# Performance work log

Measured on AMD Instinct MI355X. Metric: run time of the kernel, lower is better.

Reference implementation:

```python
import jax, jax.numpy as jnp
import numpy as np

N, D_IN, D_OUT = 100000, 256, 256
R, E, B = 8, 40000, 4
LN_EPS = 1e-5


def setup_inputs() -> dict:
    key = jax.random.key(0)
    ks = jax.random.split(key, 6)
    x = jax.random.normal(ks[0], (N, D_IN), dtype=jnp.float32)
    edge_index = jax.random.randint(ks[1], (R, 2, E), 0, N, dtype=jnp.int64)
    bases = jax.random.normal(ks[2], (B, D_IN, D_OUT), dtype=jnp.float32) * 0.01
    coefficients = jax.random.normal(ks[3], (R, B), dtype=jnp.float32) * 0.01
    bound = 1.0 / np.sqrt(D_IN)
    w_self = jax.random.uniform(ks[4], (D_IN, D_OUT), minval=-bound, maxval=bound, dtype=jnp.float32)
    b_self = jax.random.uniform(ks[5], (D_OUT,), minval=-bound, maxval=bound, dtype=jnp.float32)
    ln_gamma = jnp.ones((D_OUT,), dtype=jnp.float32)
    ln_beta = jnp.zeros((D_OUT,), dtype=jnp.float32)
    return {"x": x, "edge_index": edge_index, "bases": bases,
            "coefficients": coefficients, "w_self": w_self, "b_self": b_self,
            "ln_gamma": ln_gamma, "ln_beta": ln_beta}


def reference(x, edge_index, bases, coefficients, w_self, b_self, ln_gamma, ln_beta):
    n = x.shape[0]
    # self loop
    h = x @ w_self + b_self                                   # (N, D_OUT)
    # basis-composed per-relation weights
    W = jnp.einsum('rb,bio->rio', coefficients, bases)        # (R, D_IN, D_OUT)
    src = edge_index[:, 0]                                    # (R, E)
    dst = edge_index[:, 1]                                    # (R, E)
    msg = jnp.einsum('red,rdo->reo', x[src], W)               # (R, E, D_OUT)
    seg = jax.vmap(lambda d, m: jax.ops.segment_sum(m, d, num_segments=n))(dst, msg)
    deg = jax.vmap(lambda d: jax.ops.segment_sum(jnp.ones(d.shape, x.dtype), d, num_segments=n))(dst)
    deg = jnp.maximum(deg, 1.0)                               # clamp(min=1)
    h = h + (seg / deg[..., None]).sum(axis=0)
    # LayerNorm(SiLU(h)); dropout is identity in eval
    a = jax.nn.silu(h)
    mean = a.mean(axis=-1, keepdims=True)
    var = ((a - mean) ** 2).mean(axis=-1, keepdims=True)
    return (a - mean) * jax.lax.rsqrt(var + LN_EPS) * ln_gamma + ln_beta
```

## Files before the change

kernel.cpp:

```cpp
#include <hip/hip_runtime.h>
#include <hip/hip_bf16.h>

#define N_NODES 100000
#define D 256
#define R_REL 8
#define E_EDGES 40000
#define LN_EPS 1e-5f
#define ETOT (R_REL * E_EDGES)
#define SCAN_CH 1024
#define SCAN_NB ((N_NODES + SCAN_CH - 1) / SCAN_CH)
#define NROWT ((N_NODES + 127) / 128)
#define NWG (NROWT * 10)
#define PREPX_NB (N_NODES * D / 8 / 256)
#define PREPB_NB 80
#define COUNT_NB ((ETOT + 255) / 256)

typedef __attribute__((ext_vector_type(8))) short short8;
typedef __attribute__((ext_vector_type(4))) float f32x4;
typedef __attribute__((ext_vector_type(2))) float f32x2;
typedef unsigned char uchar;

__device__ inline ushort bf16u(float f) {
    __hip_bfloat16 h = __float2bfloat16(f);
    return *reinterpret_cast<ushort*>(&h);
}
__device__ inline float bf2f(ushort u) { return __uint_as_float(((unsigned)u) << 16); }

__global__ __launch_bounds__(256) void k_prep(const float* __restrict__ x,
                                              ushort* __restrict__ xb,
                                              const float* __restrict__ w_self,
                                              const float* __restrict__ bases,
                                              ushort* __restrict__ BT,
                                              const int* __restrict__ ei,
                                              int* __restrict__ cntR) {
    __shared__ float tile[64][65];
    int b = blockIdx.x;
    int t = threadIdx.x;
    if (b < PREPX_NB) {
        size_t idx = (size_t)b * 256 + t;
        const float4* xp = (const float4*)(x + idx * 8);
        float4 f0 = xp[0], f1 = xp[1];
        short8 v;
        v[0] = (short)bf16u(f0.x); v[1] = (short)bf16u(f0.y);
        v[2] = (short)bf16u(f0.z); v[3] = (short)bf16u(f0.w);
        v[4] = (short)bf16u(f1.x); v[5] = (short)bf16u(f1.y);
        v[6] = (short)bf16u(f1.z); v[7] = (short)bf16u(f1.w);
        *(short8*)(xb + idx * 8) = v;
    } else if (b < PREPX_NB + PREPB_NB) {
        int bb = b - PREPX_NB;
        int ot = bb >> 2, dt = bb & 3;
        int o0 = ot * 64, d0 = dt * 64;
        int m = o0 >> 8;
        const float* src = (m == 0) ? w_self : bases + (size_t)(m - 1) * D * D;
        int ol0 = o0 & 255;
        int cl = t & 63, rw = t >> 6;
        for (int i = 0; i < 16; ++i) {
            int dl = i * 4 + rw;
            tile[dl][cl] = src[(size_t)(d0 + dl) * D + ol0 + cl];
        }
        __syncthreads();
        for (int i = 0; i < 16; ++i) {
            int ol = i * 4 + rw;
            BT[(size_t)(o0 + ol) * D + d0 + cl] = bf16u(tile[cl][ol]);
        }
    } else {
        int idx = (b - PREPX_NB - PREPB_NB) * 256 + t;
        if (idx < ETOT) {
            int r = idx / E_EDGES, e = idx % E_EDGES;
            int dst = ei[(r * 2 + 1) * E_EDGES + e];
            atomicAdd(&cntR[(size_t)dst * 8 + r], 1);
        }
    }
}

__global__ __launch_bounds__(256) void k_scanA(const int* __restrict__ cntR,
                                               int* __restrict__ start,
                                               int* __restrict__ sumsA) {
    __shared__ int sc[256];
    int t = threadIdx.x;
    int base = blockIdx.x * SCAN_CH + t * 4;
    int v[4];
#pragma unroll
    for (int i = 0; i < 4; ++i) {
        int node = base + i;
        int s = 0;
        if (node < N_NODES) {
            const int4* c = (const int4*)&cntR[(size_t)node * 8];
            int4 a = c[0], b = c[1];
            s = a.x + a.y + a.z + a.w + b.x + b.y + b.z + b.w;
        }
        v[i] = s;
    }
    int ts = v[0] + v[1] + v[2] + v[3];
    sc[t] = ts;
    __syncthreads();
    for (int off = 1; off < 256; off <<= 1) {
        int val = (t >= off) ? sc[t - off] : 0;
        __syncthreads();
        sc[t] += val;
        __syncthreads();
    }
    int excl = sc[t] - ts;
    if (base + 0 < N_NODES) start[base + 0] = excl;
    if (base + 1 < N_NODES) start[base + 1] = excl + v[0];
    if (base + 2 < N_NODES) start[base + 2] = excl + v[0] + v[1];
    if (base + 3 < N_NODES) start[base + 3] = excl + v[0] + v[1] + v[2];
    if (t == 255) sumsA[blockIdx.x] = sc[255];
}

__global__ __launch_bounds__(256) void k_scanB(const int* __restrict__ sumsA,
                                               int* __restrict__ sumsB) {
    __shared__ int sc[256];
    int t = threadIdx.x;
    int i0 = t * 4;
    int v0 = (i0 + 0 < SCAN_NB) ? sumsA[i0 + 0] : 0;
    int v1 = (i0 + 1 < SCAN_NB) ? sumsA[i0 + 1] : 0;
    int v2 = (i0 + 2 < SCAN_NB) ? sumsA[i0 + 2] : 0;
    int v3 = (i0 + 3 < SCAN_NB) ? sumsA[i0 + 3] : 0;
    int ts = v0 + v1 + v2 + v3;
    sc[t] = ts;
    __syncthreads();
    for (int off = 1; off < 256; off <<= 1) {
        int val = (t >= off) ? sc[t - off] : 0;
        __syncthreads();
        sc[t] += val;
        __syncthreads();
    }
    int excl = sc[t] - ts;
    if (i0 + 0 < SCAN_NB) sumsB[i0 + 0] = excl;
    if (i0 + 1 < SCAN_NB) sumsB[i0 + 1] = excl + v0;
    if (i0 + 2 < SCAN_NB) sumsB[i0 + 2] = excl + v0 + v1;
    if (i0 + 3 < SCAN_NB) sumsB[i0 + 3] = excl + v0 + v1 + v2;
}

__global__ __launch_bounds__(256) void k_scanC(int* __restrict__ start,
                                               const int* __restrict__ sumsB,
                                               int* __restrict__ cursor) {
    int idx = blockIdx.x * blockDim.x + threadIdx.x;
    if (idx < N_NODES) {
        int v = start[idx] + sumsB[idx / SCAN_CH];
        start[idx] = v;
        cursor[idx] = v;
    }
    if (idx == 0) start[N_NODES] = ETOT;
}

__global__ void k_scatter(const int* __restrict__ ei, int* __restrict__ cursor,
                          const int* __restrict__ cntR, int2* __restrict__ pairs) {
    int idx = blockIdx.x * blockDim.x + threadIdx.x;
    if (idx >= ETOT) return;
    int r = idx / E_EDGES, e = idx % E_EDGES;
    int src = ei[r * 2 * E_EDGES + e];
    int dst = ei[(r * 2 + 1) * E_EDGES + e];
    int pos = atomicAdd(&cursor[dst], 1);
    float invd = __builtin_amdgcn_rcpf((float)cntR[(size_t)dst * 8 + r]) * 0.015625f;
    pairs[pos] = make_int2((r << 20) | src, __float_as_int(invd));
}

__global__ __launch_bounds__(256, 2) void k_gemm(const ushort* __restrict__ xb,
                                                 const ushort* __restrict__ BT,
                                                 ushort* __restrict__ hb,
                                                 uchar* __restrict__ U) {
    __shared__ ushort As[2][128 * 64];
    __shared__ ushort Bs[2][128 * 64];
    int t = threadIdx.x;

    const int q = NWG / 8, r8 = NWG % 8;
    int dd = blockIdx.x;
    int xcd = dd & 7, slot = dd >> 3;
    int wgid = (xcd < r8 ? xcd * (q + 1) : r8 * (q + 1) + (xcd - r8) * q) + slot;
    int rowtile = wgid / 10, pass = wgid % 10;
    int row0 = rowtile * 128;

    int l = t & 63, w = t >> 6;
    int wr = w >> 1, wc = w & 1;
    int lr = l & 15, lg = l >> 4;

    auto stageA = [&](int buf, int kt) {
#pragma unroll
        for (int p = 0; p < 4; ++p) {
            int o = p * 4096 + t * 16;
            int rowA = o >> 7;
            int colb = (o & 127) ^ ((rowA & 7) << 4);
            int srcrow = min(row0 + rowA, N_NODES - 1);
            const char* gp = (const char*)xb + ((size_t)srcrow * D + kt * 64) * 2 + colb;
            char* lp = (char*)&As[buf][0] + p * 4096 + (t >> 6) * 1024;
            __builtin_amdgcn_global_load_lds(
                (const __attribute__((address_space(1))) void*)gp,
                (__attribute__((address_space(3))) void*)lp, 16, 0, 0);
        }
    };
    auto stageB = [&](int buf, int kt) {
#pragma unroll
        for (int p = 0; p < 4; ++p) {
            int o = p * 4096 + t * 16;
            int rowB = o >> 7;
            int colb = (o & 127) ^ ((rowB & 7) << 4);
            const char* gp = (const char*)BT +
                ((size_t)(pass * 128 + rowB) * D + kt * 64) * 2 + colb;
            char* lp = (char*)&Bs[buf][0] + p * 4096 + (t >> 6) * 1024;
            __builtin_amdgcn_global_load_lds(
                (const __attribute__((address_space(1))) void*)gp,
                (__attribute__((address_space(3))) void*)lp, 16, 0, 0);
        }
    };

    f32x4 acc[4][4] = {};
    stageA(0, 0); stageB(0, 0);
    int buf = 0;
    for (int kt = 0; kt < 4; ++kt) {
        __syncthreads();
        if (kt < 3) { stageA(buf ^ 1, kt + 1); stageB(buf ^ 1, kt + 1); }
#pragma unroll
        for (int kk = 0; kk < 2; ++kk) {
            int kb = kk * 64 + lg * 16;
            short8 a[4], b[4];
#pragma unroll
            for (int mi = 0; mi < 4; ++mi) {
                int row = wr * 64 + mi * 16 + lr;
                a[mi] = *(const short8*)((const char*)&As[buf][0] +
                         row * 128 + (kb ^ ((row & 7) << 4)));
            }
#pragma unroll
            for (int ni = 0; ni < 4; ++ni) {
                int rb = wc * 64 + ni * 16 + lr;
                b[ni] = *(const short8*)((const char*)&Bs[buf][0] +
                         rb * 128 + (kb ^ ((rb & 7) << 4)));
            }
#pragma unroll
            for (int mi = 0; mi < 4; ++mi)
#pragma unroll
                for (int ni = 0; ni < 4; ++ni)
                    acc[mi][ni] = __builtin_amdgcn_mfma_f32_16x16x32_bf16(
                        a[mi], b[ni], acc[mi][ni], 0, 0, 0);
        }
        buf ^= 1;
    }

    if (pass < 2) {
        int qbase = pass * 128 + wc * 64 + lr * 4;
#pragma unroll
        for (int mi = 0; mi < 4; ++mi)
#pragma unroll
            for (int j = 0; j < 4; ++j) {
                int node = row0 + wr * 64 + mi * 16 + lg * 4 + j;
                if (node < N_NODES) {
                    ushort4 v4;
                    v4.x = bf16u(acc[mi][0][j]);
                    v4.y = bf16u(acc[mi][1][j]);
                    v4.z = bf16u(acc[mi][2][j]);
                    v4.w = bf16u(acc[mi][3][j]);
                    *(ushort4*)&hb[(size_t)node * D + qbase] = v4;
                }
            }
    } else {
        int pl = pass - 2;
        int qbase = (pl >> 1) * 256 + (pl & 1) * 128 + wc * 64 + lr * 4;
#pragma unroll
        for (int mi = 0; mi < 4; ++mi)
#pragma unroll
            for (int j = 0; j < 4; ++j) {
                int node = row0 + wr * 64 + mi * 16 + lg * 4 + j;
                if (node < N_NODES) {
                    unsigned d = __builtin_amdgcn_cvt_pk_fp8_f32(
                        acc[mi][0][j] * 64.0f, acc[mi][1][j] * 64.0f, 0, false);
                    d = __builtin_amdgcn_cvt_pk_fp8_f32(
                        acc[mi][2][j] * 64.0f, acc[mi][3][j] * 64.0f, d, true);
                    *(unsigned*)&U[(size_t)node * 1024 + qbase] = d;
                }
            }
    }
}

__global__ __launch_bounds__(256) void k_final(float* __restrict__ out,
                                               const ushort* __restrict__ hb,
                                               const uchar* __restrict__ U,
                                               const int* __restrict__ start,
                                               const int2* __restrict__ pairs,
                                               const float* __restrict__ coeff,
                                               const float* __restrict__ bias,
                                               const float* __restrict__ gamma,
                                               const float* __restrict__ beta) {
    __shared__ float cf[32];
    int t = threadIdx.x;
    if (t < 32) cf[t] = coeff[t];
    __syncthreads();
    int lane = t & 63, w = t >> 6;
    int n = blockIdx.x * 4 + w;
    int s = start[n], e = start[n + 1];

    int c0 = (lane >> 4) * 64 + (lane & 15);
    size_t rowo = (size_t)n * D;
    ushort4 hu = *(const ushort4*)&hb[rowo + lane * 4];
    float bb0 = bias[c0], bb1 = bias[c0 + 16], bb2 = bias[c0 + 32], bb3 = bias[c0 + 48];

    f32x2 a01 = {0.f, 0.f}, a23 = {0.f, 0.f};
    const uchar* Ul = U + lane * 4;
    int p = s;
    for (; p + 1 < e; p += 2) {
        int2 cA = pairs[p], cB = pairs[p + 1];
        const uchar* upA = Ul + ((size_t)(cA.x & 0xFFFFF) << 10);
        const uchar* upB = Ul + ((size_t)(cB.x & 0xFFFFF) << 10);
        unsigned vA0 = *(const unsigned*)(upA);
        unsigned vA1 = *(const unsigned*)(upA + 256);
        unsigned vA2 = *(const unsigned*)(upA + 512);
        unsigned vA3 = *(const unsigned*)(upA + 768);
        unsigned vB0 = *(const unsigned*)(upB);
        unsigned vB1 = *(const unsigned*)(upB + 256);
        unsigned vB2 = *(const unsigned*)(upB + 512);
        unsigned vB3 = *(const unsigned*)(upB + 768);
        float invA = __int_as_float(cA.y);
        float invB = __int_as_float(cB.y);
        const float* wvA = &cf[(cA.x >> 20) * 4];
        const float* wvB = &cf[(cB.x >> 20) * 4];
        f32x2 wp;
        float ww;
        ww = wvA[0] * invA; wp[0] = ww; wp[1] = ww;
        a01 += wp * __builtin_amdgcn_cvt_pk_f32_fp8(vA0, false);
        a23 += wp * __builtin_amdgcn_cvt_pk_f32_fp8(vA0, true);
        ww = wvA[1] * invA; wp[0] = ww; wp[1] = ww;
        a01 += wp * __builtin_amdgcn_cvt_pk_f32_fp8(vA1, false);
        a23 += wp * __builtin_amdgcn_cvt_pk_f32_fp8(vA1, true);
        ww = wvA[2] * invA; wp[0] = ww; wp[1] = ww;
        a01 += wp * __builtin_amdgcn_cvt_pk_f32_fp8(vA2, false);
        a23 += wp * __builtin_amdgcn_cvt_pk_f32_fp8(vA2, true);
        ww = wvA[3] * invA; wp[0] = ww; wp[1] = ww;
        a01 += wp * __builtin_amdgcn_cvt_pk_f32_fp8(vA3, false);
        a23 += wp * __builtin_amdgcn_cvt_pk_f32_fp8(vA3, true);
        ww = wvB[0] * invB; wp[0] = ww; wp[1] = ww;
        a01 += wp * __builtin_amdgcn_cvt_pk_f32_fp8(vB0, false);
        a23 += wp * __builtin_amdgcn_cvt_pk_f32_fp8(vB0, true);
        ww = wvB[1] * invB; wp[0] = ww; wp[1] = ww;
        a01 += wp * __builtin_amdgcn_cvt_pk_f32_fp8(vB1, false);
        a23 += wp * __builtin_amdgcn_cvt_pk_f32_fp8(vB1, true);
        ww = wvB[2] * invB; wp[0] = ww; wp[1] = ww;
        a01 += wp * __builtin_amdgcn_cvt_pk_f32_fp8(vB2, false);
        a23 += wp * __builtin_amdgcn_cvt_pk_f32_fp8(vB2, true);
        ww = wvB[3] * invB; wp[0] = ww; wp[1] = ww;
        a01 += wp * __builtin_amdgcn_cvt_pk_f32_fp8(vB3, false);
        a23 += wp * __builtin_amdgcn_cvt_pk_f32_fp8(vB3, true);
    }
    if (p < e) {
        int2 cA = pairs[p];
        const uchar* upA = Ul + ((size_t)(cA.x & 0xFFFFF) << 10);
        unsigned vA0 = *(const unsigned*)(upA);
        unsigned vA1 = *(const unsigned*)(upA + 256);
        unsigned vA2 = *(const unsigned*)(upA + 512);
        unsigned vA3 = *(const unsigned*)(upA + 768);
        float invA = __int_as_float(cA.y);
        const float* wvA = &cf[(cA.x >> 20) * 4];
        f32x2 wp;
        float ww;
        ww = wvA[0] * invA; wp[0] = ww; wp[1] = ww;
        a01 += wp * __builtin_amdgcn_cvt_pk_f32_fp8(vA0, false);
        a23 += wp * __builtin_amdgcn_cvt_pk_f32_fp8(vA0, true);
        ww = wvA[1] * invA; wp[0] = ww; wp[1] = ww;
        a01 += wp * __builtin_amdgcn_cvt_pk_f32_fp8(vA1, false);
        a23 += wp * __builtin_amdgcn_cvt_pk_f32_fp8(vA1, true);
        ww = wvA[2] * invA; wp[0] = ww; wp[1] = ww;
        a01 += wp * __builtin_amdgcn_cvt_pk_f32_fp8(vA2, false);
        a23 += wp * __builtin_amdgcn_cvt_pk_f32_fp8(vA2, true);
        ww = wvA[3] * invA; wp[0] = ww; wp[1] = ww;
        a01 += wp * __builtin_amdgcn_cvt_pk_f32_fp8(vA3, false);
        a23 += wp * __builtin_amdgcn_cvt_pk_f32_fp8(vA3, true);
    }

    float a[4];
    a[0] = bf2f(hu.x) + bb0 + a01[0];
    a[1] = bf2f(hu.y) + bb1 + a01[1];
    a[2] = bf2f(hu.z) + bb2 + a23[0];
    a[3] = bf2f(hu.w) + bb3 + a23[1];
    float sum = 0.f, sq = 0.f;
#pragma unroll
    for (int j = 0; j < 4; ++j) {
        float ex = __expf(-a[j]);
        a[j] = a[j] * __builtin_amdgcn_rcpf(1.f + ex);
        sum += a[j]; sq += a[j] * a[j];
    }
#pragma unroll
    for (int off = 32; off >= 1; off >>= 1) {
        sum += __shfl_xor(sum, off, 64);
        sq  += __shfl_xor(sq,  off, 64);
    }
    float mean = sum * (1.0f / 256.0f);
    float var = sq * (1.0f / 256.0f) - mean * mean;
    float rs = rsqrtf(var + LN_EPS);
#pragma unroll
    for (int j = 0; j < 4; ++j) {
        int c = c0 + j * 16;
        out[rowo + c] = (a[j] - mean) * rs * gamma[c] + beta[c];
    }
}

extern "C" void kernel_launch(void* const* d_in, const int* in_sizes, int n_in,
                              void* d_out, int out_size, void* d_ws, size_t ws_size,
                              hipStream_t stream) {
    const float* x      = (const float*)d_in[0];
    const int*   ei     = (const int*)d_in[1];
    const float* bases  = (const float*)d_in[2];
    const float* coeff  = (const float*)d_in[3];
    const float* w_self = (const float*)d_in[4];
    const float* b_self = (const float*)d_in[5];
    const float* gamma  = (const float*)d_in[6];
    const float* beta   = (const float*)d_in[7];
    float* out = (float*)d_out;

    ushort* BT  = (ushort*)d_ws;
    ushort* xb  = BT + (size_t)1280 * D;
    ushort* hb  = xb + (size_t)N_NODES * D;
    uchar*  U   = (uchar*)(hb + (size_t)N_NODES * D);
    int* cntR   = (int*)(U + (size_t)N_NODES * 1024);
    int* start  = cntR + (size_t)R_REL * N_NODES;
    int* cursor = start + N_NODES + 1;
    int* sumsA  = cursor + N_NODES;
    int* sumsB  = sumsA + 128;
    int2* pairs = (int2*)(sumsB + 128);

    hipMemsetAsync(cntR, 0, (size_t)R_REL * N_NODES * sizeof(int), stream);

    k_prep<<<PREPX_NB + PREPB_NB + COUNT_NB, 256, 0, stream>>>(x, xb, w_self,
                                                               bases, BT, ei, cntR);
    k_scanA<<<SCAN_NB, 256, 0, stream>>>(cntR, start, sumsA);
    k_scanB<<<1, 256, 0, stream>>>(sumsA, sumsB);
    k_scanC<<<(N_NODES + 255) / 256, 256, 0, stream>>>(start, sumsB, cursor);
    k_scatter<<<(ETOT + 255) / 256, 256, 0, stream>>>(ei, cursor, cntR, pairs);
    k_gemm<<<NWG, 256, 0, stream>>>(xb, BT, hb, U);
    k_final<<<N_NODES / 4, 256, 0, stream>>>(out, hb, U, start, pairs, coeff,
                                             b_self, gamma, beta);
}
```

Baseline: 238.3 us.

## Shrink GEMM K-tile to 32 with k-major LDS layout to raise occupancy

Halves the K tile of the bf16 MFMA GEMM from 64 to 32, which halves shared memory per block and allows launch bounds of 5 workgroups per CU instead of 2. The LDS tile layout moves from XOR-swizzled row-major to k-slice-major, so each lane's 16-byte fragment reads are contiguous without swizzle math. In exchange there are twice as many K iterations and barriers, each doing half the MFMA work, and the higher occupancy target may force register spills given the 64 accumulator registers.

```diff
diff --git a/kernel.cpp b/kernel.cpp
--- a/kernel.cpp
+++ b/kernel.cpp
@@ -157,12 +157,12 @@
     pairs[pos] = make_int2((r << 20) | src, __float_as_int(invd));
 }
 
-__global__ __launch_bounds__(256, 2) void k_gemm(const ushort* __restrict__ xb,
+__global__ __launch_bounds__(256, 5) void k_gemm(const ushort* __restrict__ xb,
                                                  const ushort* __restrict__ BT,
                                                  ushort* __restrict__ hb,
                                                  uchar* __restrict__ U) {
-    __shared__ ushort As[2][128 * 64];
-    __shared__ ushort Bs[2][128 * 64];
+    __shared__ ushort As[2][128 * 32];
+    __shared__ ushort Bs[2][128 * 32];
     int t = threadIdx.x;
 
     const int q = NWG / 8, r8 = NWG % 8;
@@ -178,12 +178,12 @@
 
     auto stageA = [&](int buf, int kt) {
 #pragma unroll
-        for (int p = 0; p < 4; ++p) {
-            int o = p * 4096 + t * 16;
-            int rowA = o >> 7;
-            int colb = (o & 127) ^ ((rowA & 7) << 4);
-            int srcrow = min(row0 + rowA, N_NODES - 1);
-            const char* gp = (const char*)xb + ((size_t)srcrow * D + kt * 64) * 2 + colb;
+        for (int p = 0; p < 2; ++p) {
+            int c = p * 256 + t;
+            int row = c & 127, ks = c >> 7;
+            int srcrow = min(row0 + row, N_NODES - 1);
+            const char* gp = (const char*)xb +
+                ((size_t)srcrow * D + kt * 32 + ks * 8) * 2;
             char* lp = (char*)&As[buf][0] + p * 4096 + (t >> 6) * 1024;
             __builtin_amdgcn_global_load_lds(
                 (const __attribute__((address_space(1))) void*)gp,
@@ -192,12 +192,11 @@
     };
     auto stageB = [&](int buf, int kt) {
 #pragma unroll
-        for (int p = 0; p < 4; ++p) {
-            int o = p * 4096 + t * 16;
-            int rowB = o >> 7;
-            int colb = (o & 127) ^ ((rowB & 7) << 4);
+        for (int p = 0; p < 2; ++p) {
+            int c = p * 256 + t;
+            int row = c & 127, ks = c >> 7;
             const char* gp = (const char*)BT +
-                ((size_t)(pass * 128 + rowB) * D + kt * 64) * 2 + colb;
+                ((size_t)(pass * 128 + row) * D + kt * 32 + ks * 8) * 2;
             char* lp = (char*)&Bs[buf][0] + p * 4096 + (t >> 6) * 1024;
             __builtin_amdgcn_global_load_lds(
                 (const __attribute__((address_space(1))) void*)gp,
@@ -208,32 +207,25 @@
     f32x4 acc[4][4] = {};
     stageA(0, 0); stageB(0, 0);
     int buf = 0;
-    for (int kt = 0; kt < 4; ++kt) {
-        __syncthreads();
-        if (kt < 3) { stageA(buf ^ 1, kt + 1); stageB(buf ^ 1, kt + 1); }
-#pragma unroll
-        for (int kk = 0; kk < 2; ++kk) {
-            int kb = kk * 64 + lg * 16;
-            short8 a[4], b[4];
-#pragma unroll
-            for (int mi = 0; mi < 4; ++mi) {
-                int row = wr * 64 + mi * 16 + lr;
-                a[mi] = *(const short8*)((const char*)&As[buf][0] +
-                         row * 128 + (kb ^ ((row & 7) << 4)));
-            }
-#pragma unroll
-            for (int ni = 0; ni < 4; ++ni) {
-                int rb = wc * 64 + ni * 16 + lr;
-                b[ni] = *(const short8*)((const char*)&Bs[buf][0] +
-                         rb * 128 + (kb ^ ((rb & 7) << 4)));
-            }
-#pragma unroll
-            for (int mi = 0; mi < 4; ++mi)
-#pragma unroll
-                for (int ni = 0; ni < 4; ++ni)
-                    acc[mi][ni] = __builtin_amdgcn_mfma_f32_16x16x32_bf16(
-                        a[mi], b[ni], acc[mi][ni], 0, 0, 0);
-        }
+    for (int kt = 0; kt < 8; ++kt) {
+        __syncthreads();
+        if (kt < 7) { stageA(buf ^ 1, kt + 1); stageB(buf ^ 1, kt + 1); }
+        int koff = lg * 2048;
+        short8 a[4], b[4];
+#pragma unroll
+        for (int mi = 0; mi < 4; ++mi)
+            a[mi] = *(const short8*)((const char*)&As[buf][0] +
+                     koff + (wr * 64 + mi * 16 + lr) * 16);
+#pragma unroll
+        for (int ni = 0; ni < 4; ++ni)
+            b[ni] = *(const short8*)((const char*)&Bs[buf][0] +
+                     koff + (wc * 64 + ni * 16 + lr) * 16);
+#pragma unroll
+        for (int mi = 0; mi < 4; ++mi)
+#pragma unroll
+            for (int ni = 0; ni < 4; ++ni)
+                acc[mi][ni] = __builtin_amdgcn_mfma_f32_16x16x32_bf16(
+                    a[mi], b[ni], acc[mi][ni], 0, 0, 0);
         buf ^= 1;
     }
 
```

After: 309.0 us. 29.7% more time.
